# Performance work log

Hardware: AMD Instinct MI355X
Metric: run time of the kernel (lower is better)

The kernel has to match this reference:

```python
import jax, jax.numpy as jnp
import numpy as np

B, H, W = 64, 128, 128
PS, G = 8, 16            # patch size, token grid (128//8)
E = 256                  # embed_dim (hidden_dim)
NS, IT, TEMP = 8, 3, 1.0 # num_slots, slot_iters, slot_temperature
V = 10                   # vocab_size
FD = 320                 # full_dim = latent_dim(256) + pose_dim(64)
HEADS, HD = 4, E // 4    # RoPE attn heads / head_dim
N = G * G


def _ln(x, g, b, eps=1e-5):
    m = x.mean(-1, keepdims=True)
    v = ((x - m) ** 2).mean(-1, keepdims=True)
    return (x - m) * jax.lax.rsqrt(v + eps) * g + b


def _conv(x, w, stride):
    return jax.lax.conv_general_dilated(
        x, w, (stride, stride), 'VALID',
        dimension_numbers=('NCHW', 'OIHW', 'NCHW'))


def _rope_tables(g, hd):
    half = hd // 2
    inv = 1.0 / (10000.0 ** (jnp.arange(0, half, 2, dtype=jnp.float32) / half))
    pos = jnp.arange(g, dtype=jnp.float32)
    p = jnp.outer(pos, inv)                                  # [g, half//2]
    e = jnp.concatenate([jnp.sin(p), jnp.cos(p)], axis=-1)   # [g, half]
    ex = jnp.broadcast_to(e[None, :, :], (g, g, half))
    ey = jnp.broadcast_to(e[:, None, :], (g, g, half))
    emb = jnp.concatenate([ey, ex], axis=-1).reshape(g * g, hd)
    return jnp.cos(emb)[None, :, None, :], jnp.sin(emb)[None, :, None, :]


def _apply_rope(x, cos, sin):
    x1, x2 = x[..., 0::2], x[..., 1::2]
    rot = jnp.concatenate([-x2, x1], axis=-1)
    return x * cos + rot * sin


def _gru(x, h, wih, whh, bih, bhh):
    gi = x @ wih.T + bih
    gh = h @ whh.T + bhh
    i_r, i_z, i_n = jnp.split(gi, 3, axis=-1)
    h_r, h_z, h_n = jnp.split(gh, 3, axis=-1)
    r = jax.nn.sigmoid(i_r + h_r)
    z = jax.nn.sigmoid(i_z + h_z)
    n = jnp.tanh(i_n + r * h_n)
    return (1.0 - z) * n + z * h


def setup_inputs() -> dict:
    key = jax.random.key(0)
    ks = iter(jax.random.split(key, 40))

    def nrm(shape, s=0.02):
        return (jax.random.normal(next(ks), shape, jnp.float32) * s)

    state = jax.random.randint(next(ks), (B, 1, H, W), 0, V).astype(jnp.float32)
    return {
        'state': state,
        'conv_w': nrm((E, 12, PS, PS)), 'conv_b': jnp.zeros((E,), jnp.float32),
        'mlp_ln_g': jnp.ones((E,), jnp.float32), 'mlp_ln_b': jnp.zeros((E,), jnp.float32),
        'mlp_w1': nrm((2 * E, E)), 'mlp_b1': jnp.zeros((2 * E,), jnp.float32),
        'mlp_w2': nrm((E, 2 * E)), 'mlp_b2': jnp.zeros((E,), jnp.float32),
        'qkv_w': nrm((3 * E, E)), 'qkv_b': jnp.zeros((3 * E,), jnp.float32),
        'proj_w': nrm((E, E)), 'proj_b': jnp.zeros((E,), jnp.float32),
        'ni_g': jnp.ones((E,), jnp.float32), 'ni_b': jnp.zeros((E,), jnp.float32),
        'ns_g': jnp.ones((FD,), jnp.float32), 'ns_b': jnp.zeros((FD,), jnp.float32),
        'nm_g': jnp.ones((FD,), jnp.float32), 'nm_b': jnp.zeros((FD,), jnp.float32),
        'q_w': nrm((FD, FD)), 'k_w': nrm((FD, E)), 'v_w': nrm((FD, E)),
        'gru_wih': nrm((3 * FD, FD)), 'gru_whh': nrm((3 * FD, FD)),
        'gru_bih': jnp.zeros((3 * FD,), jnp.float32), 'gru_bhh': jnp.zeros((3 * FD,), jnp.float32),
        'smlp_w1': nrm((2 * FD, FD)), 'smlp_b1': jnp.zeros((2 * FD,), jnp.float32),
        'smlp_w2': nrm((FD, 2 * FD)), 'smlp_b2': jnp.zeros((FD,), jnp.float32),
    }


def reference(state, conv_w, conv_b, mlp_ln_g, mlp_ln_b, mlp_w1, mlp_b1,
              mlp_w2, mlp_b2, qkv_w, qkv_b, proj_w, proj_b, ni_g, ni_b,
              ns_g, ns_b, nm_g, nm_b, q_w, k_w, v_w,
              gru_wih, gru_whh, gru_bih, gru_bhh,
              smlp_w1, smlp_b1, smlp_w2, smlp_b2):
    # Sobel edge features on replicate-padded image
    sob_x = jnp.array([[-1., 0., 1.], [-2., 0., 2.], [-1., 0., 1.]], jnp.float32).reshape(1, 1, 3, 3)
    sob_y = jnp.array([[-1., -2., -1.], [0., 0., 0.], [1., 2., 1.]], jnp.float32).reshape(1, 1, 3, 3)
    pad = jnp.pad(state, ((0, 0), (0, 0), (1, 1), (1, 1)), mode='edge')
    sx = _conv(pad, sob_x, 1)
    sy = _conv(pad, sob_y, 1)
    ids = jax.lax.stop_gradient(state)[:, 0].astype(jnp.int32)
    onehot = jax.nn.one_hot(ids, V, dtype=jnp.float32).transpose(0, 3, 1, 2)
    comp = jnp.concatenate([onehot, sx, sy], axis=1)            # [B,12,H,W]

    # Patch embed -> tokens [B,N,E]
    x = _conv(comp, conv_w, PS) + conv_b[None, :, None, None]   # [B,E,G,G]
    x = x.reshape(B, E, N).transpose(0, 2, 1)

    # patch_mlp (LN -> Linear -> GELU -> Linear), no residual
    h = _ln(x, mlp_ln_g, mlp_ln_b)
    h = jax.nn.gelu(h @ mlp_w1.T + mlp_b1, approximate=False)
    x = h @ mlp_w2.T + mlp_b2

    # RoPE self-attention, residual
    cos, sin = _rope_tables(G, HD)
    qkv = (x @ qkv_w.T + qkv_b).reshape(B, N, 3, HEADS, HD)
    q, k, v = qkv[:, :, 0], qkv[:, :, 1], qkv[:, :, 2]          # [B,N,Hh,HD]
    q = _apply_rope(q, cos, sin).transpose(0, 2, 1, 3)          # [B,Hh,N,HD]
    k = _apply_rope(k, cos, sin).transpose(0, 2, 1, 3)
    v = v.transpose(0, 2, 1, 3)
    attn = jax.nn.softmax(jnp.einsum('bhnd,bhmd->bhnm', q, k) * HD ** -0.5, axis=-1)
    ao = jnp.einsum('bhnm,bhmd->bhnd', attn, v).transpose(0, 2, 1, 3).reshape(B, N, E)
    x = x + (ao @ proj_w.T + proj_b)
    x = _ln(x, ni_g, ni_b)

    k_in = x @ k_w.T                                            # [B,N,FD]
    v_in = x @ v_w.T

    # No codebook injected -> zero slot priors
    slots = jnp.zeros((B, NS, FD), jnp.float32)
    sattn = None
    for _ in range(IT):
        slots_prev = slots
        q_s = _ln(slots, ns_g, ns_b) @ q_w.T                    # [B,NS,FD]
        logits = jnp.einsum('bnf,bsf->bns', k_in, q_s) * FD ** -0.5
        sattn = jax.nn.softmax(logits / TEMP, axis=-1)          # over slots
        an = sattn + 1e-8
        an = an / an.sum(axis=1, keepdims=True)                 # normalize over keys
        updates = jnp.einsum('bns,bnf->bsf', an, v_in)          # [B,NS,FD]
        slots = _gru(updates.reshape(-1, FD), slots_prev.reshape(-1, FD),
                     gru_wih, gru_whh, gru_bih, gru_bhh).reshape(B, NS, FD)
        m = _ln(slots, nm_g, nm_b)
        m = jax.nn.gelu(m @ smlp_w1.T + smlp_b1, approximate=False)
        slots = slots + (m @ smlp_w2.T + smlp_b2)

    masks = jax.lax.stop_gradient(sattn).transpose(0, 2, 1).reshape(B, NS, G, G)
    return slots, masks
```

## Files before the change

kernel.cpp:

```cpp
#include <hip/hip_runtime.h>
#include <math.h>

#define BB   64
#define HH   128
#define WW   128
#define GG   16
#define NN   256
#define EE   256
#define FD   320
#define NSL  8
#define NHEAD 4
#define HD   64
#define KIM  768

using short8 = __attribute__((ext_vector_type(8))) short;
using f32x4  = __attribute__((ext_vector_type(4))) float;

__device__ __forceinline__ float sigm(float x) { return 1.0f / (1.0f + expf(-x)); }
__device__ __forceinline__ float gelu_exact(float x) {
    return 0.5f * x * (1.0f + erff(x * 0.70710678118654752f));
}
__device__ __forceinline__ unsigned short f2b(float x) {
    unsigned u = __float_as_uint(x);
    u += 0x7fffu + ((u >> 16) & 1u);
    return (unsigned short)(u >> 16);
}
__device__ __forceinline__ float b2f(unsigned short u) {
    return __uint_as_float(((unsigned)u) << 16);
}
__device__ __forceinline__ void gload_lds16(const void* g, void* lds) {
    __builtin_amdgcn_global_load_lds(
        (const __attribute__((address_space(1))) unsigned int*)g,
        (__attribute__((address_space(3))) unsigned int*)lds, 16, 0, 0);
}
__device__ __forceinline__ void store_el(float* p, float v) { *p = v; }
__device__ __forceinline__ void store_el(unsigned short* p, float v) { *p = f2b(v); }

__global__ __launch_bounds__(256) void cvt_weights(
    const float* __restrict__ w0, const float* __restrict__ w1,
    const float* __restrict__ w2, const float* __restrict__ w3,
    const float* __restrict__ w4, const float* __restrict__ w5,
    const float* __restrict__ w6, const float* __restrict__ w7,
    const float* __restrict__ w8, const float* __restrict__ w9,
    const float* __restrict__ w10, const float* __restrict__ w11,
    unsigned short* __restrict__ dst) {
    int i = blockIdx.x * 256 + threadIdx.x;
    float v;
    if      (i <  196608) v = w0[i];
    else if (i <  327680) v = w1[i - 196608];
    else if (i <  458752) v = w2[i - 327680];
    else if (i <  655360) v = w3[i - 458752];
    else if (i <  720896) v = w4[i - 655360];
    else if (i <  802816) v = w5[i - 720896];
    else if (i <  884736) v = w6[i - 802816];
    else if (i <  987136) v = w7[i - 884736];
    else if (i < 1294336) v = w8[i - 987136];
    else if (i < 1601536) v = w9[i - 1294336];
    else if (i < 1806336) v = w10[i - 1601536];
    else                  v = w11[i - 1806336];
    dst[i] = f2b(v);
}

__global__ __launch_bounds__(256) void cvt_bf16(const float* __restrict__ in,
                                                unsigned short* __restrict__ out, int n) {
    int i = blockIdx.x * 256 + threadIdx.x;
    if (i < n) out[i] = f2b(in[i]);
}

__global__ __launch_bounds__(256) void rope_tab(float* __restrict__ cs,
                                                float* __restrict__ sn) {
    int i = blockIdx.x * 256 + threadIdx.x;
    int d = i & 63, n = i >> 6;
    int pos = (d < 32) ? (n >> 4) : (n & 15);
    int j = d & 31;
    float freq = powf(10000.0f, -(float)(j & 15) / 16.0f);
    float p = (float)pos * freq;
    float ang = (j < 16) ? sinf(p) : cosf(p);
    cs[i] = cosf(ang);
    sn[i] = sinf(ang);
}

__global__ __launch_bounds__(256) void sobel_im2col(const float* __restrict__ state,
                                                    unsigned short* __restrict__ X0) {
    int idx = blockIdx.x * 256 + threadIdx.x;
    if (idx >= BB * HH * WW) return;
    int w = idx % WW;
    int h = (idx / WW) % HH;
    int b = idx / (HH * WW);
    const float* st = state + (long)b * HH * WW;
    auto at = [&](int y, int x) {
        y = min(max(y, 0), HH - 1);
        x = min(max(x, 0), WW - 1);
        return st[y * WW + x];
    };
    float v00 = at(h-1, w-1), v01 = at(h-1, w), v02 = at(h-1, w+1);
    float v10 = at(h,   w-1),                  v12 = at(h,   w+1);
    float v20 = at(h+1, w-1), v21 = at(h+1, w), v22 = at(h+1, w+1);
    float sx = (v02 - v00) + 2.0f * (v12 - v10) + (v22 - v20);
    float sy = (v20 - v00) + 2.0f * (v21 - v01) + (v22 - v02);
    int id = (int)st[h * WW + w];
    int gy = h >> 3, i = h & 7, gx = w >> 3, j = w & 7;
    long row = (long)b * NN + gy * GG + gx;
    unsigned short* xr = X0 + row * KIM + i * 8 + j;
#pragma unroll
    for (int c = 0; c < 10; c++) xr[c * 64] = (id == c) ? 0x3F80u : 0u;
    xr[10 * 64] = f2b(sx);
    xr[11 * 64] = f2b(sy);
}

template <int BM, int BN, int ACT>
__global__ __launch_bounds__(256) void gemm_bf16(
    const unsigned short* __restrict__ A, const unsigned short* __restrict__ W,
    const float* __restrict__ bias, const float* __restrict__ res,
    float* __restrict__ C, unsigned short* __restrict__ Cb,
    int K, long sA, long sW, long sC1, long sC2, int cdiv, int ldc, float scale)
{
    constexpr int WN = BN / 64;
    __shared__ __align__(16) unsigned short As[BM * 32];
    __shared__ __align__(16) unsigned short Bs[BN * 32];
    const int tid = threadIdx.x;
    const int w = tid >> 6, l = tid & 63;
    const int wm = w / WN, wn = w % WN;
    const int bz = blockIdx.z;
    const unsigned short* Ab = A + (long)bz * sA + (long)(blockIdx.y * BM) * K;
    const unsigned short* Wb = W + (long)bz * sW + (long)(blockIdx.x * BN) * K;
    const long offC = (long)(bz / cdiv) * sC1 + (long)(bz % cdiv) * sC2;

    const int rA  = l >> 2;
    const int swz = ((l & 3) ^ ((l >> 3) & 3)) * 8;

    f32x4 acc[4][4] = {};

    for (int k0 = 0; k0 < K; k0 += 32) {
#pragma unroll
        for (int c = 0; c < BM / 64; c++) {
            const int chunk = w * (BM / 64) + c;
            gload_lds16(Ab + (long)(chunk * 16 + rA) * K + k0 + swz, (char*)As + chunk * 1024);
        }
#pragma unroll
        for (int c = 0; c < BN / 64; c++) {
            const int chunk = w * (BN / 64) + c;
            gload_lds16(Wb + (long)(chunk * 16 + rA) * K + k0 + swz, (char*)Bs + chunk * 1024);
        }
        __syncthreads();
        short8 af[4], bfr[4];
#pragma unroll
        for (int m = 0; m < 4; m++) {
            const int row = wm * 64 + m * 16 + (l & 15);
            const int byte = row * 64 + (((l >> 4) ^ ((row >> 1) & 3)) << 4);
            af[m] = *(const short8*)((const char*)As + byte);
        }
#pragma unroll
        for (int n = 0; n < 4; n++) {
            const int row = wn * 64 + n * 16 + (l & 15);
            const int byte = row * 64 + (((l >> 4) ^ ((row >> 1) & 3)) << 4);
            bfr[n] = *(const short8*)((const char*)Bs + byte);
        }
#pragma unroll
        for (int m = 0; m < 4; m++)
#pragma unroll
            for (int n = 0; n < 4; n++)
                acc[m][n] = __builtin_amdgcn_mfma_f32_16x16x32_bf16(af[m], bfr[n], acc[m][n], 0, 0, 0);
        __syncthreads();
    }

    const int crow0 = blockIdx.y * BM + wm * 64;
    const int ccol0 = blockIdx.x * BN + wn * 64;
#pragma unroll
    for (int m = 0; m < 4; m++) {
#pragma unroll
        for (int n = 0; n < 4; n++) {
            const int row = crow0 + m * 16 + ((l >> 4) << 2);
            const int col = ccol0 + n * 16 + (l & 15);
#pragma unroll
            for (int r = 0; r < 4; r++) {
                float v = acc[m][n][r] * scale;
                if (bias) v += bias[col];
                if (ACT == 1) v = gelu_exact(v);
                const long idx = offC + (long)(row + r) * ldc + col;
                if (res) v += res[idx];
                if (C)  C[idx] = v;
                if (Cb) Cb[idx] = f2b(v);
            }
        }
    }
}

template <int ACT>
__global__ __launch_bounds__(256) void gemm_bf16_s(
    const unsigned short* __restrict__ A, const unsigned short* __restrict__ W,
    const float* __restrict__ bias0, const float* __restrict__ bias1,
    const float* __restrict__ res,
    float* __restrict__ C, unsigned short* __restrict__ Cb,
    int K, int N, long sA, long sW, long sC, float scale)
{
    __shared__ __align__(16) unsigned short As[64 * 32];
    __shared__ __align__(16) unsigned short Bs[64 * 32];
    const int tid = threadIdx.x;
    const int w = tid >> 6, l = tid & 63;
    const int gw = l >> 4, l15 = l & 15;
    const int bz = blockIdx.z;
    const unsigned short* Ab = A + (long)bz * sA + (long)(blockIdx.y * 64) * K;
    const unsigned short* Wb = W + (long)bz * sW + (long)(blockIdx.x * 64) * K;
    const float* bias = (bz == 0) ? bias0 : bias1;
    const long offC = (long)bz * sC;

    const int rA  = l >> 2;
    const int swz = ((l & 3) ^ ((l >> 3) & 3)) * 8;

    f32x4 acc[4] = {};

    for (int k0 = 0; k0 < K; k0 += 32) {
        gload_lds16(Ab + (long)(w * 16 + rA) * K + k0 + swz, (char*)As + w * 1024);
        gload_lds16(Wb + (long)(w * 16 + rA) * K + k0 + swz, (char*)Bs + w * 1024);
        __syncthreads();
        short8 af[4];
#pragma unroll
        for (int m = 0; m < 4; m++) {
            const int row = m * 16 + l15;
            af[m] = *(const short8*)((const char*)As + row * 64 + ((gw ^ ((row >> 1) & 3)) << 4));
        }
        const int brow = w * 16 + l15;
        const short8 bf = *(const short8*)((const char*)Bs + brow * 64 + ((gw ^ ((brow >> 1) & 3)) << 4));
#pragma unroll
        for (int m = 0; m < 4; m++)
            acc[m] = __builtin_amdgcn_mfma_f32_16x16x32_bf16(af[m], bf, acc[m], 0, 0, 0);
        __syncthreads();
    }

    const int col = blockIdx.x * 64 + w * 16 + l15;
    const int row0 = blockIdx.y * 64;
#pragma unroll
    for (int m = 0; m < 4; m++) {
        const int row = row0 + m * 16 + (gw << 2);
#pragma unroll
        for (int r = 0; r < 4; r++) {
            float v = acc[m][r] * scale;
            if (bias) v += bias[col];
            if (ACT == 1) v = gelu_exact(v);
            const long idx = offC + (long)(row + r) * N + col;
            if (res) v += res[idx];
            if (C)  C[idx] = v;
            if (Cb) Cb[idx] = f2b(v);
        }
    }
}

template <typename OT>
__global__ __launch_bounds__(256) void ln_rows(const float* __restrict__ X,
                                               OT* __restrict__ Y,
                                               const float* __restrict__ g,
                                               const float* __restrict__ b,
                                               int rows, int D) {
    int gtid = blockIdx.x * 256 + threadIdx.x;
    int row = gtid >> 6;
    int lane = gtid & 63;
    if (row >= rows) return;
    const float* x = X + (long)row * D;
    const int nv = D >> 6;
    float v[5];
    float s = 0.0f;
#pragma unroll 5
    for (int i = 0; i < nv; i++) { v[i] = x[lane + (i << 6)]; s += v[i]; }
#pragma unroll
    for (int o = 32; o; o >>= 1) s += __shfl_down(s, o);
    s = __shfl(s, 0);
    float mean = s / (float)D;
    float s2 = 0.0f;
#pragma unroll 5
    for (int i = 0; i < nv; i++) { float d = v[i] - mean; s2 += d * d; }
#pragma unroll
    for (int o = 32; o; o >>= 1) s2 += __shfl_down(s2, o);
    s2 = __shfl(s2, 0);
    float inv = rsqrtf(s2 / (float)D + 1e-5f);
    OT* y = Y + (long)row * D;
#pragma unroll 5
    for (int i = 0; i < nv; i++) {
        int d = lane + (i << 6);
        store_el(&y[d], (v[i] - mean) * inv * g[d] + b[d]);
    }
}

__global__ __launch_bounds__(256) void gru_ln(const float* __restrict__ GI,
                                              const float* __restrict__ GH,
                                              float* __restrict__ slots,
                                              const float* __restrict__ g,
                                              const float* __restrict__ b,
                                              unsigned short* __restrict__ SLnb) {
    int gtid = blockIdx.x * 256 + threadIdx.x;
    int row = gtid >> 6;
    int lane = gtid & 63;
    const float* gi = GI + (long)row * 960;
    const float* gh = GH + (long)row * 960;
    float* sl = slots + (long)row * FD;
    float h[5];
    float s = 0.0f;
#pragma unroll
    for (int i = 0; i < 5; i++) {
        const int f = lane + (i << 6);
        const float rr = sigm(gi[f] + gh[f]);
        const float z  = sigm(gi[320 + f] + gh[320 + f]);
        const float nn = tanhf(gi[640 + f] + rr * gh[640 + f]);
        const float hn = (1.0f - z) * nn + z * sl[f];
        h[i] = hn;
        s += hn;
        sl[f] = hn;
    }
#pragma unroll
    for (int o = 32; o; o >>= 1) s += __shfl_down(s, o);
    s = __shfl(s, 0);
    const float mean = s * (1.0f / FD);
    float s2 = 0.0f;
#pragma unroll
    for (int i = 0; i < 5; i++) { const float d = h[i] - mean; s2 += d * d; }
#pragma unroll
    for (int o = 32; o; o >>= 1) s2 += __shfl_down(s2, o);
    s2 = __shfl(s2, 0);
    const float inv = rsqrtf(s2 * (1.0f / FD) + 1e-5f);
    unsigned short* y = SLnb + (long)row * FD;
#pragma unroll
    for (int i = 0; i < 5; i++) {
        const int f = lane + (i << 6);
        y[f] = f2b((h[i] - mean) * inv * g[f] + b[f]);
    }
}

__global__ __launch_bounds__(256) void rope_qk(const unsigned short* __restrict__ QKVb,
                                               const float* __restrict__ cs,
                                               const float* __restrict__ sn,
                                               unsigned short* __restrict__ Qr,
                                               unsigned short* __restrict__ Kr) {
    const int rid = blockIdx.x * 256 + threadIdx.x;
    const int n = rid & 255;
    const int h = (rid >> 8) & 3;
    const int b = rid >> 10;
    const unsigned short* src = QKVb + ((long)(b * 256 + n)) * 768 + h * 64;
    float cv[64], sv[64];
#pragma unroll
    for (int i = 0; i < 16; i++) {
        *(float4*)&cv[i * 4] = *(const float4*)(cs + n * 64 + i * 4);
        *(float4*)&sv[i * 4] = *(const float4*)(sn + n * 64 + i * 4);
    }
#pragma unroll
    for (int qk = 0; qk < 2; qk++) {
        const unsigned short* s0 = src + qk * 256;
        unsigned short* dst = (qk == 0 ? Qr : Kr) + (long)rid * 64;
        float x[64];
#pragma unroll
        for (int i = 0; i < 8; i++) {
            short8 v = *(const short8*)(s0 + i * 8);
#pragma unroll
            for (int j = 0; j < 8; j++) x[i * 8 + j] = b2f((unsigned short)v[j]);
        }
        unsigned short o[64];
#pragma unroll
        for (int d = 0; d < 64; d++) {
            const float rot = (d < 32) ? -x[2 * d + 1] : x[2 * (d - 32)];
            o[d] = f2b(x[d] * cv[d] + rot * sv[d]);
        }
#pragma unroll
        for (int i = 0; i < 8; i++)
            *(short8*)(dst + i * 8) = *(short8*)&o[i * 8];
    }
}

__global__ __launch_bounds__(256, 1) void fused_attn(
    const unsigned short* __restrict__ Qr,
    const unsigned short* __restrict__ Kr,
    const unsigned short* __restrict__ QKVb,
    unsigned short* __restrict__ AOb)
{
    __shared__ __align__(16) char SL[49152];
    const int h = blockIdx.x, b = blockIdx.y;
    const int tid = threadIdx.x;
    const int w = tid >> 6, l = tid & 63;
    const int gw = l >> 4, l15 = l & 15;
    const long bh = (long)b * 4 + h;
    const unsigned short* Qb = Qr + bh * NN * 64;
    const unsigned short* Kb = Kr + bh * NN * 64;

    {
        const int n0 = (tid & 127) * 2;
        const int dh = tid >> 7;
        const unsigned short* v0p = QKVb + ((long)b * NN + n0) * 768 + h * 64 + 512 + dh * 32;
        const unsigned short* v1p = v0p + 768;
        unsigned short v0[32], v1[32];
#pragma unroll
        for (int i = 0; i < 4; i++) {
            *(short8*)&v0[i * 8] = *(const short8*)(v0p + i * 8);
            *(short8*)&v1[i * 8] = *(const short8*)(v1p + i * 8);
        }
#pragma unroll
        for (int i = 0; i < 32; i++) {
            const int d = dh * 32 + i;
            const unsigned val = (unsigned)v0[i] | ((unsigned)v1[i] << 16);
            *(unsigned*)(SL + d * 512 + (((n0 >> 3) ^ (d & 15)) << 4) + (n0 & 7) * 2) = val;
        }
    }
    __syncthreads();

    char* Pw = SL + 32768 + w * 4096;

#pragma unroll
    for (int p = 0; p < 2; p++) {
        const int mbase = w * 64 + p * 32;
        f32x4 accs[16][2] = {};
#pragma unroll
        for (int kk = 0; kk < 2; kk++) {
            short8 bq[2];
#pragma unroll
            for (int mf = 0; mf < 2; mf++)
                bq[mf] = *(const short8*)(Qb + ((mbase + mf * 16 + l15) << 6) + kk * 32 + gw * 8);
#pragma unroll
            for (int nf = 0; nf < 16; nf++) {
                const short8 ak = *(const short8*)(Kb + ((nf * 16 + l15) << 6) + kk * 32 + gw * 8);
#pragma unroll
                for (int mf = 0; mf < 2; mf++)
                    accs[nf][mf] = __builtin_amdgcn_mfma_f32_16x16x32_bf16(ak, bq[mf], accs[nf][mf], 0, 0, 0);
            }
        }
        float rs[2];
#pragma unroll
        for (int mf = 0; mf < 2; mf++) {
            float mx = -1e30f;
#pragma unroll
            for (int nf = 0; nf < 16; nf++)
#pragma unroll
                for (int r = 0; r < 4; r++) mx = fmaxf(mx, accs[nf][mf][r]);
            mx = fmaxf(mx, __shfl_xor(mx, 16));
            mx = fmaxf(mx, __shfl_xor(mx, 32));
            float sum = 0.0f;
#pragma unroll
            for (int nf = 0; nf < 16; nf++)
#pragma unroll
                for (int r = 0; r < 4; r++) {
                    const float e = expf((accs[nf][mf][r] - mx) * 0.125f);
                    accs[nf][mf][r] = e;
                    sum += e;
                }
            sum += __shfl_xor(sum, 16);
            sum += __shfl_xor(sum, 32);
            rs[mf] = 1.0f / sum;
        }
        f32x4 acco[4][2] = {};
#pragma unroll
        for (int c = 0; c < 4; c++) {
#pragma unroll
            for (int nfi = 0; nfi < 4; nfi++) {
                const int nf = c * 4 + nfi;
                const int kt = nf >> 1;
                const int gr = (nf & 1) * 2 + (gw >> 1);
                const int lr = l15 + 16 * gr;
                const int j0 = (gw & 1) * 4;
#pragma unroll
                for (int mf = 0; mf < 2; mf++) {
                    uint2 pk;
                    pk.x = (unsigned)f2b(accs[nf][mf][0] * rs[mf]) |
                           ((unsigned)f2b(accs[nf][mf][1] * rs[mf]) << 16);
                    pk.y = (unsigned)f2b(accs[nf][mf][2] * rs[mf]) |
                           ((unsigned)f2b(accs[nf][mf][3] * rs[mf]) << 16);
                    *(uint2*)(Pw + ((kt & 1) * 2 + mf) * 1024 + lr * 16 + j0 * 2) = pk;
                }
            }
#pragma unroll
            for (int kti = 0; kti < 2; kti++) {
                const int kt = c * 2 + kti;
                short8 vf[4];
#pragma unroll
                for (int df = 0; df < 4; df++) {
                    const int d = df * 16 + l15;
                    vf[df] = *(const short8*)(SL + d * 512 + (((kt * 4 + gw) ^ (d & 15)) << 4));
                }
#pragma unroll
                for (int mf = 0; mf < 2; mf++) {
                    const short8 pf = *(const short8*)(Pw + (kti * 2 + mf) * 1024 + l * 16);
#pragma unroll
                    for (int df = 0; df < 4; df++)
                        acco[df][mf] = __builtin_amdgcn_mfma_f32_16x16x32_bf16(vf[df], pf, acco[df][mf], 0, 0, 0);
                }
            }
        }
#pragma unroll
        for (int df = 0; df < 4; df++)
#pragma unroll
            for (int mf = 0; mf < 2; mf++) {
                const int m = mbase + mf * 16 + l15;
                const int d = df * 16 + gw * 4;
                unsigned short o[4];
#pragma unroll
                for (int r = 0; r < 4; r++) o[r] = f2b(acco[df][mf][r]);
                *(uint2*)(AOb + ((long)(b * NN + m) * 256 + h * 64 + d)) = *(uint2*)o;
            }
    }
}

__global__ __launch_bounds__(256) void slot_logits(const float* __restrict__ Kin,
                                                   const float* __restrict__ Qs,
                                                   float* __restrict__ sattn,
                                                   float* __restrict__ sums) {
    const int b = blockIdx.x;
    const int chunk = blockIdx.y;
    __shared__ float qs[NSL][FD];
    __shared__ float colsum[NSL];
    const int tid = threadIdx.x;
    for (int i = tid; i < NSL * FD; i += 256) qs[i / FD][i % FD] = Qs[(long)b * NSL * FD + i];
    if (tid < NSL) colsum[tid] = 0.0f;
    __syncthreads();
    const int wv = tid >> 6, lane = tid & 63;
    float wsum[NSL] = {};
#pragma unroll
    for (int rr = 0; rr < 4; rr++) {
        const int r = chunk * 16 + wv * 4 + rr;
        const float* kr = Kin + ((long)b * NN + r) * FD;
        float acc[NSL] = {};
#pragma unroll
        for (int i = 0; i < 5; i++) {
            const int t = lane + (i << 6);
            const float kv = kr[t];
#pragma unroll
            for (int s = 0; s < NSL; s++) acc[s] = fmaf(kv, qs[s][t], acc[s]);
        }
#pragma unroll
        for (int s = 0; s < NSL; s++)
#pragma unroll
            for (int o = 32; o; o >>= 1) acc[s] += __shfl_down(acc[s], o);
        if (lane == 0) {
            const float scale = 0.055901699437494740f;
            float mx = -1e30f;
#pragma unroll
            for (int s = 0; s < NSL; s++) { acc[s] *= scale; mx = fmaxf(mx, acc[s]); }
            float e[NSL], sum = 0.0f;
#pragma unroll
            for (int s = 0; s < NSL; s++) { e[s] = expf(acc[s] - mx); sum += e[s]; }
            const float rsum = 1.0f / sum;
            float* outp = sattn + ((long)b * NN + r) * NSL;
#pragma unroll
            for (int s = 0; s < NSL; s++) {
                const float pp = e[s] * rsum;
                outp[s] = pp;
                wsum[s] += pp;
            }
        }
    }
    if (lane == 0) {
#pragma unroll
        for (int s = 0; s < NSL; s++) atomicAdd(&colsum[s], wsum[s]);
    }
    __syncthreads();
    if (tid < NSL) atomicAdd(&sums[b * NSL + tid], colsum[tid]);
}

__global__ __launch_bounds__(256) void slot_updates(const float* __restrict__ sattn,
                                                    const float* __restrict__ sums,
                                                    const float* __restrict__ Vin,
                                                    float* __restrict__ Upd) {
    const int b = blockIdx.x;
    const int chunk = blockIdx.y;
    const int t = threadIdx.x;
    __shared__ float an[64][NSL];
    __shared__ float inv_s[NSL];
    if (t < NSL) inv_s[t] = 1.0f / (sums[b * NSL + t] + (float)NN * 1e-8f);
    __syncthreads();
    for (int i = t; i < 64 * NSL; i += 256) {
        const int s = i & 7;
        const int n = i >> 3;
        an[n][s] = (sattn[((long)b * NN + chunk * 64 + n) * NSL + s] + 1e-8f) * inv_s[s];
    }
    __syncthreads();
    float acc[NSL][2] = {};
    const float* vb = Vin + ((long)b * NN + chunk * 64) * FD;
    for (int n = 0; n < 64; n++) {
        const float v1 = vb[(long)n * FD + t];
        const float v2 = (t < 64) ? vb[(long)n * FD + 256 + t] : 0.0f;
#pragma unroll
        for (int s = 0; s < NSL; s++) {
            const float a = an[n][s];
            acc[s][0] = fmaf(a, v1, acc[s][0]);
            acc[s][1] = fmaf(a, v2, acc[s][1]);
        }
    }
    float* ub = Upd + (long)b * NSL * FD;
#pragma unroll
    for (int s = 0; s < NSL; s++) {
        atomicAdd(&ub[s * FD + t], acc[s][0]);
        if (t < 64) atomicAdd(&ub[s * FD + 256 + t], acc[s][1]);
    }
}

__global__ __launch_bounds__(256) void write_out(const float* __restrict__ slots,
                                                 const float* __restrict__ sattn,
                                                 float* __restrict__ out) {
    int idx = blockIdx.x * 256 + threadIdx.x;
    const int SLOT_SZ = BB * NSL * FD;
    const int MASK_SZ = BB * NSL * NN;
    if (idx < SLOT_SZ) {
        out[idx] = slots[idx];
    } else if (idx < SLOT_SZ + MASK_SZ) {
        int i = idx - SLOT_SZ;
        int b = i >> 11;
        int s = (i >> 8) & 7;
        int n = i & 255;
        out[idx] = sattn[((long)b * NN + n) * NSL + s];
    }
}

extern "C" void kernel_launch(void* const* d_in, const int* in_sizes, int n_in,
                              void* d_out, int out_size, void* d_ws, size_t ws_size,
                              hipStream_t stream) {
    const float* state    = (const float*)d_in[0];
    const float* conv_w   = (const float*)d_in[1];
    const float* conv_b   = (const float*)d_in[2];
    const float* mlp_ln_g = (const float*)d_in[3];
    const float* mlp_ln_b = (const float*)d_in[4];
    const float* mlp_w1   = (const float*)d_in[5];
    const float* mlp_b1   = (const float*)d_in[6];
    const float* mlp_w2   = (const float*)d_in[7];
    const float* mlp_b2   = (const float*)d_in[8];
    const float* qkv_w    = (const float*)d_in[9];
    const float* qkv_b    = (const float*)d_in[10];
    const float* proj_w   = (const float*)d_in[11];
    const float* proj_b   = (const float*)d_in[12];
    const float* ni_g     = (const float*)d_in[13];
    const float* ni_b     = (const float*)d_in[14];
    const float* ns_g     = (const float*)d_in[15];
    const float* ns_b     = (const float*)d_in[16];
    const float* nm_g     = (const float*)d_in[17];
    const float* nm_b     = (const float*)d_in[18];
    const float* q_w      = (const float*)d_in[19];
    const float* k_w      = (const float*)d_in[20];
    const float* v_w      = (const float*)d_in[21];
    const float* gru_wih  = (const float*)d_in[22];
    const float* gru_whh  = (const float*)d_in[23];
    const float* gru_bih  = (const float*)d_in[24];
    const float* gru_bhh  = (const float*)d_in[25];
    const float* smlp_w1  = (const float*)d_in[26];
    const float* smlp_b1  = (const float*)d_in[27];
    const float* smlp_w2  = (const float*)d_in[28];
    const float* smlp_b2  = (const float*)d_in[29];

    float* ws = (float*)d_ws;
    const int M = BB * NN;
    typedef unsigned short u16;

    u16*   X0b  = (u16*)(ws + 0L);
    u16*   Qr   = (u16*)(ws + 0L);
    u16*   Kr   = (u16*)(ws + 2097152L);
    float* X1   = ws + 6291456L;
    u16*   XLNb = (u16*)(ws + 10485760L);
    u16*   Hbufb= (u16*)(ws + 12582912L);
    u16*   QKVb = (u16*)(ws + 6291456L);
    u16*   X2b  = (u16*)(ws + 23068672L);
    float* X2   = ws + 31457280L;
    u16*   Xnb  = (u16*)(ws + 31457280L);
    float* X3   = ws + 35651584L;
    float* Slots= ws + 35651584L;
    float* Qs   = ws + 35979264L;
    float* Satt = ws + 36143104L;
    float* Sums = ws + 36274176L;
    float* Upd  = ws + 36274688L;
    float* GI   = ws + 36438528L;
    float* GH   = ws + 36930048L;
    u16*   SLnb = (u16*)(ws + 37421568L);
    u16*   Updb = (u16*)(ws + 37503488L);
    u16*   Slotsb=(u16*)(ws + 37585408L);
    u16*   Mhb  = (u16*)(ws + 37667328L);
    float* Kin  = ws + 39845888L;
    float* Vin  = ws + 45088768L;
    u16*   AOb    = (u16*)(ws + 50331648L);
    u16*   wb     = (u16*)(ws + 52428800L);
    u16*   conv_wb= wb + 0;
    u16*   mlp_w1b= wb + 196608;
    u16*   mlp_w2b= wb + 327680;
    u16*   qkv_wb = wb + 458752;
    u16*   proj_wb= wb + 655360;
    u16*   k_wb   = wb + 720896;
    u16*   v_wb   = wb + 802816;
    u16*   q_wb   = wb + 884736;
    u16*   wihb   = wb + 987136;
    u16*   whhb   = wb + 1294336;
    u16*   smlp1b = wb + 1601536;
    u16*   smlp2b = wb + 1806336;
    float* CS     = ws + 53434368L;
    float* SN     = ws + 53450752L;

    float* out = (float*)d_out;

    auto gemmA = [&](const u16* A, const u16* Wt, const float* bias, const float* res,
                     float* C, u16* Cb, int Mm, int Nn, int Kk, int batch,
                     long sA, long sW, long sC1, long sC2, int cdiv, int ldc,
                     float scale, int act) {
        dim3 grid(Nn / 128, Mm / 128, batch);
        if (act) gemm_bf16<128, 128, 1><<<grid, 256, 0, stream>>>(A, Wt, bias, res, C, Cb, Kk, sA, sW, sC1, sC2, cdiv, ldc, scale);
        else     gemm_bf16<128, 128, 0><<<grid, 256, 0, stream>>>(A, Wt, bias, res, C, Cb, Kk, sA, sW, sC1, sC2, cdiv, ldc, scale);
    };
    auto gemmB = [&](const u16* A, const u16* Wt, float* C, int Mm, int Nn, int Kk) {
        dim3 grid(Nn / 64, Mm / 256, 1);
        gemm_bf16<256, 64, 0><<<grid, 256, 0, stream>>>(A, Wt, nullptr, nullptr, C, nullptr, Kk, 0, 0, 0, 0, 1, Nn, 1.0f);
    };
    auto gemmS = [&](const u16* A, const u16* Wt, const float* b0, const float* b1,
                     const float* res, float* C, u16* Cb, int Mm, int Nn, int Kk,
                     int batch, long sA, long sW, long sC, int act) {
        dim3 grid(Nn / 64, Mm / 64, batch);
        if (act) gemm_bf16_s<1><<<grid, 256, 0, stream>>>(A, Wt, b0, b1, res, C, Cb, Kk, Nn, sA, sW, sC, 1.0f);
        else     gemm_bf16_s<0><<<grid, 256, 0, stream>>>(A, Wt, b0, b1, res, C, Cb, Kk, Nn, sA, sW, sC, 1.0f);
    };

    cvt_weights<<<dim3(2011136 / 256), 256, 0, stream>>>(conv_w, mlp_w1, mlp_w2, qkv_w,
                                                         proj_w, k_w, v_w, q_w,
                                                         gru_wih, gru_whh, smlp_w1, smlp_w2, wb);
    rope_tab<<<dim3(16384 / 256), 256, 0, stream>>>(CS, SN);

    sobel_im2col<<<dim3((BB * HH * WW) / 256), 256, 0, stream>>>(state, X0b);
    gemmA(X0b, conv_wb, conv_b, nullptr, X1, nullptr, M, EE, KIM, 1, 0, 0, 0, 0, 1, EE, 1.0f, 0);
    ln_rows<u16><<<dim3(M * 64 / 256), 256, 0, stream>>>(X1, XLNb, mlp_ln_g, mlp_ln_b, M, EE);
    gemmA(XLNb, mlp_w1b, mlp_b1, nullptr, nullptr, Hbufb, M, 2 * EE, EE, 1, 0, 0, 0, 0, 1, 2 * EE, 1.0f, 1);
    gemmA(Hbufb, mlp_w2b, mlp_b2, nullptr, X2, X2b, M, EE, 2 * EE, 1, 0, 0, 0, 0, 1, EE, 1.0f, 0);
    gemmA(X2b, qkv_wb, qkv_b, nullptr, nullptr, QKVb, M, 3 * EE, EE, 1, 0, 0, 0, 0, 1, 3 * EE, 1.0f, 0);
    rope_qk<<<dim3(65536 / 256), 256, 0, stream>>>(QKVb, CS, SN, Qr, Kr);
    fused_attn<<<dim3(NHEAD, BB), 256, 0, stream>>>(Qr, Kr, QKVb, AOb);
    gemmA(AOb, proj_wb, proj_b, X2, X3, nullptr, M, EE, EE, 1, 0, 0, 0, 0, 1, EE, 1.0f, 0);
    ln_rows<u16><<<dim3(M * 64 / 256), 256, 0, stream>>>(X3, Xnb, ni_g, ni_b, M, EE);
    gemmB(Xnb, k_wb, Kin, M, FD, EE);
    gemmB(Xnb, v_wb, Vin, M, FD, EE);
    hipMemsetAsync(Slots, 0, (size_t)BB * NSL * FD * sizeof(float), stream);
    hipMemsetAsync(Slotsb, 0, (size_t)BB * NSL * FD * sizeof(u16), stream);
    for (int it = 0; it < 3; it++) {
        ln_rows<u16><<<dim3(512 * 64 / 256), 256, 0, stream>>>(Slots, SLnb, ns_g, ns_b, 512, FD);
        gemmS(SLnb, q_wb, nullptr, nullptr, nullptr, Qs, nullptr, 512, FD, FD, 1, 0, 0, 0, 0);
        hipMemsetAsync(Sums, 0, (size_t)BB * NSL * sizeof(float), stream);
        slot_logits<<<dim3(BB, 16), 256, 0, stream>>>(Kin, Qs, Satt, Sums);
        hipMemsetAsync(Upd, 0, (size_t)BB * NSL * FD * sizeof(float), stream);
        slot_updates<<<dim3(BB, 4), 256, 0, stream>>>(Satt, Sums, Vin, Upd);
        cvt_bf16<<<dim3(163840 / 256), 256, 0, stream>>>(Upd, Updb, 163840);
        gemmS(Updb, wihb, gru_bih, gru_bhh, nullptr, GI, nullptr, 512, 960, FD,
              2, 163840, 307200, 491520, 0);
        gru_ln<<<dim3(512 * 64 / 256), 256, 0, stream>>>(GI, GH, Slots, nm_g, nm_b, SLnb);
        gemmS(SLnb, smlp1b, smlp_b1, nullptr, nullptr, nullptr, Mhb, 512, 2 * FD, FD, 1, 0, 0, 0, 1);
        gemmS(Mhb, smlp2b, smlp_b2, nullptr, Slots, Slots, Slotsb, 512, FD, 2 * FD, 1, 0, 0, 0, 0);
    }
    write_out<<<dim3((BB * NSL * FD + BB * NSL * NN + 255) / 256), 256, 0, stream>>>(Slots, Satt, out);
}
```

Before: 644.1 us.

## Fuse slot-attention reductions, drop atomics, memsets, cvt and write_out kernels

slot_logits now writes per-chunk column sums to a buffer instead of using atomics, and on the final iteration writes the transposed masks straight into the output. slot_updates runs as one block per batch: it reduces all 256 keys through shared memory and emits bf16 updates directly. This removes the Upd memset, the atomic accumulation and the separate cvt_bf16 pass. The final slot MLP GEMM writes into the output buffer, so write_out is gone. The cost is fewer blocks for slot_updates (64 instead of 256) and a large shared-memory reduction buffer (about 40KB), which lowers parallelism for that kernel.

```diff
diff --git a/kernel.cpp b/kernel.cpp
--- a/kernel.cpp
+++ b/kernel.cpp
@@ -61,12 +61,6 @@
     dst[i] = f2b(v);
 }
 
-__global__ __launch_bounds__(256) void cvt_bf16(const float* __restrict__ in,
-                                                unsigned short* __restrict__ out, int n) {
-    int i = blockIdx.x * 256 + threadIdx.x;
-    if (i < n) out[i] = f2b(in[i]);
-}
-
 __global__ __launch_bounds__(256) void rope_tab(float* __restrict__ cs,
                                                 float* __restrict__ sn) {
     int i = blockIdx.x * 256 + threadIdx.x;
@@ -497,7 +491,8 @@
 __global__ __launch_bounds__(256) void slot_logits(const float* __restrict__ Kin,
                                                    const float* __restrict__ Qs,
                                                    float* __restrict__ sattn,
-                                                   float* __restrict__ sums) {
+                                                   float* __restrict__ sums2,
+                                                   float* __restrict__ mout) {
     const int b = blockIdx.x;
     const int chunk = blockIdx.y;
     __shared__ float qs[NSL][FD];
@@ -539,6 +534,7 @@
                 const float pp = e[s] * rsum;
                 outp[s] = pp;
                 wsum[s] += pp;
+                if (mout) mout[(long)b * 2048 + s * 256 + r] = pp;
             }
         }
     }
@@ -547,60 +543,64 @@
         for (int s = 0; s < NSL; s++) atomicAdd(&colsum[s], wsum[s]);
     }
     __syncthreads();
-    if (tid < NSL) atomicAdd(&sums[b * NSL + tid], colsum[tid]);
+    if (tid < NSL) sums2[((long)(b << 4) + chunk) * NSL + tid] = colsum[tid];
 }
 
 __global__ __launch_bounds__(256) void slot_updates(const float* __restrict__ sattn,
-                                                    const float* __restrict__ sums,
+                                                    const float* __restrict__ sums2,
                                                     const float* __restrict__ Vin,
-                                                    float* __restrict__ Upd) {
+                                                    unsigned short* __restrict__ Updb) {
     const int b = blockIdx.x;
-    const int chunk = blockIdx.y;
-    const int t = threadIdx.x;
-    __shared__ float an[64][NSL];
+    const int tid = threadIdx.x;
+    const int w = tid >> 6, l = tid & 63;
     __shared__ float inv_s[NSL];
-    if (t < NSL) inv_s[t] = 1.0f / (sums[b * NSL + t] + (float)NN * 1e-8f);
+    __shared__ float an_s[NN][NSL];
+    __shared__ float red[4][NSL][FD];
+    if (tid < NSL) {
+        float tot = (float)NN * 1e-8f;
+#pragma unroll
+        for (int c = 0; c < 16; c++) tot += sums2[((long)(b << 4) + c) * NSL + tid];
+        inv_s[tid] = 1.0f / tot;
+    }
     __syncthreads();
-    for (int i = t; i < 64 * NSL; i += 256) {
-        const int s = i & 7;
-        const int n = i >> 3;
-        an[n][s] = (sattn[((long)b * NN + chunk * 64 + n) * NSL + s] + 1e-8f) * inv_s[s];
+    {
+        const float4 p0 = *(const float4*)(sattn + ((long)b * NN + tid) * NSL);
+        const float4 p1 = *(const float4*)(sattn + ((long)b * NN + tid) * NSL + 4);
+        an_s[tid][0] = (p0.x + 1e-8f) * inv_s[0];
+        an_s[tid][1] = (p0.y + 1e-8f) * inv_s[1];
+        an_s[tid][2] = (p0.z + 1e-8f) * inv_s[2];
+        an_s[tid][3] = (p0.w + 1e-8f) * inv_s[3];
+        an_s[tid][4] = (p1.x + 1e-8f) * inv_s[4];
+        an_s[tid][5] = (p1.y + 1e-8f) * inv_s[5];
+        an_s[tid][6] = (p1.z + 1e-8f) * inv_s[6];
+        an_s[tid][7] = (p1.w + 1e-8f) * inv_s[7];
     }
     __syncthreads();
-    float acc[NSL][2] = {};
-    const float* vb = Vin + ((long)b * NN + chunk * 64) * FD;
-    for (int n = 0; n < 64; n++) {
-        const float v1 = vb[(long)n * FD + t];
-        const float v2 = (t < 64) ? vb[(long)n * FD + 256 + t] : 0.0f;
-#pragma unroll
-        for (int s = 0; s < NSL; s++) {
-            const float a = an[n][s];
-            acc[s][0] = fmaf(a, v1, acc[s][0]);
-            acc[s][1] = fmaf(a, v2, acc[s][1]);
-        }
-    }
-    float* ub = Upd + (long)b * NSL * FD;
-#pragma unroll
-    for (int s = 0; s < NSL; s++) {
-        atomicAdd(&ub[s * FD + t], acc[s][0]);
-        if (t < 64) atomicAdd(&ub[s * FD + 256 + t], acc[s][1]);
-    }
-}
-
-__global__ __launch_bounds__(256) void write_out(const float* __restrict__ slots,
-                                                 const float* __restrict__ sattn,
-                                                 float* __restrict__ out) {
-    int idx = blockIdx.x * 256 + threadIdx.x;
-    const int SLOT_SZ = BB * NSL * FD;
-    const int MASK_SZ = BB * NSL * NN;
-    if (idx < SLOT_SZ) {
-        out[idx] = slots[idx];
-    } else if (idx < SLOT_SZ + MASK_SZ) {
-        int i = idx - SLOT_SZ;
-        int b = i >> 11;
-        int s = (i >> 8) & 7;
-        int n = i & 255;
-        out[idx] = sattn[((long)b * NN + n) * NSL + s];
+    float acc[NSL][5] = {};
+    const float* vb = Vin + ((long)b * NN + w * 64) * FD;
+    for (int i = 0; i < 64; i++) {
+        float v[5];
+#pragma unroll
+        for (int j = 0; j < 5; j++) v[j] = vb[(long)i * FD + l + (j << 6)];
+        float a[NSL];
+#pragma unroll
+        for (int s = 0; s < NSL; s++) a[s] = an_s[w * 64 + i][s];
+#pragma unroll
+        for (int s = 0; s < NSL; s++)
+#pragma unroll
+            for (int j = 0; j < 5; j++)
+                acc[s][j] = fmaf(a[s], v[j], acc[s][j]);
+    }
+#pragma unroll
+    for (int s = 0; s < NSL; s++)
+#pragma unroll
+        for (int j = 0; j < 5; j++)
+            red[w][s][l + (j << 6)] = acc[s][j];
+    __syncthreads();
+    for (int idx = tid; idx < NSL * FD; idx += 256) {
+        const int s = idx / FD, f = idx % FD;
+        const float tot = red[0][s][f] + red[1][s][f] + red[2][s][f] + red[3][s][f];
+        Updb[((long)b * NSL + s) * FD + f] = f2b(tot);
     }
 }
 
@@ -656,8 +656,7 @@
     float* Slots= ws + 35651584L;
     float* Qs   = ws + 35979264L;
     float* Satt = ws + 36143104L;
-    float* Sums = ws + 36274176L;
-    float* Upd  = ws + 36274688L;
+    float* Sums2= ws + 36274176L;
     float* GI   = ws + 36438528L;
     float* GH   = ws + 36930048L;
     u16*   SLnb = (u16*)(ws + 37421568L);
@@ -727,16 +726,16 @@
     for (int it = 0; it < 3; it++) {
         ln_rows<u16><<<dim3(512 * 64 / 256), 256, 0, stream>>>(Slots, SLnb, ns_g, ns_b, 512, FD);
         gemmS(SLnb, q_wb, nullptr, nullptr, nullptr, Qs, nullptr, 512, FD, FD, 1, 0, 0, 0, 0);
-        hipMemsetAsync(Sums, 0, (size_t)BB * NSL * sizeof(float), stream);
-        slot_logits<<<dim3(BB, 16), 256, 0, stream>>>(Kin, Qs, Satt, Sums);
-        hipMemsetAsync(Upd, 0, (size_t)BB * NSL * FD * sizeof(float), stream);
-        slot_updates<<<dim3(BB, 4), 256, 0, stream>>>(Satt, Sums, Vin, Upd);
-        cvt_bf16<<<dim3(163840 / 256), 256, 0, stream>>>(Upd, Updb, 163840);
+        slot_logits<<<dim3(BB, 16), 256, 0, stream>>>(Kin, Qs, Satt, Sums2,
+                                                      (it == 2) ? (out + 163840) : nullptr);
+        slot_updates<<<dim3(BB), 256, 0, stream>>>(Satt, Sums2, Vin, Updb);
         gemmS(Updb, wihb, gru_bih, gru_bhh, nullptr, GI, nullptr, 512, 960, FD,
               2, 163840, 307200, 491520, 0);
         gru_ln<<<dim3(512 * 64 / 256), 256, 0, stream>>>(GI, GH, Slots, nm_g, nm_b, SLnb);
         gemmS(SLnb, smlp1b, smlp_b1, nullptr, nullptr, nullptr, Mhb, 512, 2 * FD, FD, 1, 0, 0, 0, 1);
-        gemmS(Mhb, smlp2b, smlp_b2, nullptr, Slots, Slots, Slotsb, 512, FD, 2 * FD, 1, 0, 0, 0, 0);
-    }
-    write_out<<<dim3((BB * NSL * FD + BB * NSL * NN + 255) / 256), 256, 0, stream>>>(Slots, Satt, out);
-}
+        if (it < 2)
+            gemmS(Mhb, smlp2b, smlp_b2, nullptr, Slots, Slots, Slotsb, 512, FD, 2 * FD, 1, 0, 0, 0, 0);
+        else
+            gemmS(Mhb, smlp2b, smlp_b2, nullptr, Slots, out, nullptr, 512, FD, 2 * FD, 1, 0, 0, 0, 0);
+    }
+}
```

Measured after the change: 627.0 us. 2.7% less time.
